# Optimization experiments

Hardware: AMD Instinct MI355X
Metric: run time of the kernel (lower is better)

Reference implementation:

```python
import jax, jax.numpy as jnp
import numpy as np

RETURN_SHAPE = (128, 128)


def dht2(x):
    # Discrete Hartley Transform over the spatial axes (2, 3):
    # H = Re(FFT) - Im(FFT). Unnormalized, matching scipy.fft default.
    f = jnp.fft.fftn(x, axes=(2, 3))
    return f.real - f.imag


def setup_inputs() -> dict:
    key = jax.random.key(0)
    x = jax.random.normal(key, (8, 64, 256, 256), dtype=jnp.float32)
    return {"x": x}


def reference(x) -> jnp.ndarray:
    # Spectral pooling: DHT -> center crop in frequency domain -> DHT.
    h_out, w_out = RETURN_SHAPE
    H, W = x.shape[2], x.shape[3]
    d = dht2(x)
    sh = (H - h_out) // 2
    sw = (W - w_out) // 2
    cropped = d[:, :, sh:sh + h_out, sw:sw + w_out]
    return dht2(cropped).astype(jnp.float32)
```

## Files before the change

kernel.cpp:

```cpp
#include <hip/hip_runtime.h>
#include <math.h>


typedef __attribute__((ext_vector_type(8))) short bfrag;
typedef __attribute__((ext_vector_type(4))) float ffrag;

#define PI2_256 0.0245436926061702597f
#define PI2_128 0.0490873852123405194f

__device__ __forceinline__ unsigned short f2bf(float f) {
    union { float f; unsigned int u; } v; v.f = f;
    unsigned int r = v.u + 0x7fffu + ((v.u >> 16) & 1u);
    return (unsigned short)(r >> 16);
}

__device__ __forceinline__ bfrag pack8(float4 a, float4 b) {
    bfrag r;
    r[0] = (short)f2bf(a.x); r[1] = (short)f2bf(a.y);
    r[2] = (short)f2bf(a.z); r[3] = (short)f2bf(a.w);
    r[4] = (short)f2bf(b.x); r[5] = (short)f2bf(b.y);
    r[6] = (short)f2bf(b.z); r[7] = (short)f2bf(b.w);
    return r;
}

__global__ __launch_bounds__(256) void gen_tables(unsigned short* __restrict__ ws)
{
    const int id = blockIdx.x * 256 + threadIdx.x;
    {
        const int j = id >> 8, m = id & 255;
        const int mult = (j < 128) ? (64 + j) : (320 - j);
        const int idx = (mult * m) & 255;
        float s, c; sincosf((float)idx * PI2_256, &s, &c);
        ws[id] = f2bf(c + s);
    }
    {
        const int u = id >> 9, k = id & 511;
        const int up = 64 + u;
        float s, c, val;
        if (k < 256) { sincosf((float)((up * k) & 255) * PI2_256, &s, &c); val = c; }
        else         { sincosf((float)((up * (k - 256)) & 255) * PI2_256, &s, &c); val = s; }
        ws[65536 + id] = f2bf(val);
    }
    if (id < 32768) {
        {
            const int j = id >> 7, m = id & 127;
            const int mult = (j < 128) ? j : (256 - j);
            const int idx = (mult * m) & 127;
            float s, c; sincosf((float)idx * PI2_128, &s, &c);
            ws[131072 + id] = f2bf(c + s);
        }
        {
            const int u = id >> 8, k = id & 255;
            float s, c, val;
            if (k < 128) { sincosf((float)((u * k) & 127) * PI2_128, &s, &c); val = c; }
            else         { sincosf((float)((u * (k - 128)) & 127) * PI2_128, &s, &c); val = s; }
            ws[163840 + id] = f2bf(val);
        }
    }
}

__global__ __launch_bounds__(512, 2) void stage1(const float* __restrict__ X,
                                                 const unsigned short* __restrict__ ws,
                                                 float* __restrict__ dc)
{
    __shared__ unsigned short PQt[128 * 512];

    const int t  = threadIdx.x;
    const int w  = t >> 6;
    const int ln = t & 15;
    const int q  = (t & 63) >> 4;
    const int img = blockIdx.x;

    const float* __restrict__ Xi = X + (size_t)img * 65536;
    const unsigned short* __restrict__ W1 = ws;
    const unsigned short* __restrict__ W2 = ws + 65536;

    {
        ffrag acc[2][16];
#pragma unroll
        for (int mt = 0; mt < 2; ++mt)
#pragma unroll
            for (int nt = 0; nt < 16; ++nt)
                acc[mt][nt] = (ffrag){0.f, 0.f, 0.f, 0.f};

        const int rowA0 = 32 * w;
        for (int kk = 0; kk < 8; ++kk) {
            const int k = kk * 32 + q * 8;
            bfrag A[2];
#pragma unroll
            for (int mt = 0; mt < 2; ++mt) {
                const float* xp = Xi + (size_t)(rowA0 + 16 * mt + ln) * 256 + k;
                const float4 x0 = *(const float4*)xp;
                const float4 x1 = *(const float4*)(xp + 4);
                A[mt] = pack8(x0, x1);
            }
#pragma unroll
            for (int nt = 0; nt < 16; ++nt) {
                const int j = nt * 16 + ln;
                const bfrag B = *(const bfrag*)(W1 + j * 256 + k);
#pragma unroll
                for (int mt = 0; mt < 2; ++mt)
                    acc[mt][nt] = __builtin_amdgcn_mfma_f32_16x16x32_bf16(A[mt], B, acc[mt][nt], 0, 0, 0);
            }
        }
#pragma unroll
        for (int mt = 0; mt < 2; ++mt) {
#pragma unroll
            for (int nt = 0; nt < 16; ++nt) {
                const int c  = nt * 16 + ln;
                const int v  = c & 127;
                const int kb = ((c < 128) ? 0 : 256) + rowA0 + 16 * mt + 4 * q;
                const unsigned int lo = (unsigned int)f2bf(acc[mt][nt][0]) |
                                        ((unsigned int)f2bf(acc[mt][nt][1]) << 16);
                const unsigned int hi = (unsigned int)f2bf(acc[mt][nt][2]) |
                                        ((unsigned int)f2bf(acc[mt][nt][3]) << 16);
                const int phys = v * 512 + ((((kb >> 3) ^ (v & 7)) << 3)) + (kb & 7);
                *(uint2*)&PQt[phys] = make_uint2(lo, hi);
            }
        }
    }
    __syncthreads();

    {
        ffrag acc[8];
#pragma unroll
        for (int nt = 0; nt < 8; ++nt) acc[nt] = (ffrag){0.f, 0.f, 0.f, 0.f};

        const int u0 = 16 * w;
        for (int kk = 0; kk < 16; ++kk) {
            const int k = kk * 32 + q * 8;
            const bfrag A = *(const bfrag*)(W2 + (size_t)(u0 + ln) * 512 + k);
#pragma unroll
            for (int nt = 0; nt < 8; ++nt) {
                const int v = nt * 16 + ln;
                const int g = (k >> 3) ^ (v & 7);
                const bfrag B = *(const bfrag*)&PQt[v * 512 + (g << 3)];
                acc[nt] = __builtin_amdgcn_mfma_f32_16x16x32_bf16(A, B, acc[nt], 0, 0, 0);
            }
        }
        float* __restrict__ D = dc + (size_t)img * 16384;
#pragma unroll
        for (int nt = 0; nt < 8; ++nt) {
#pragma unroll
            for (int r = 0; r < 4; ++r) {
                const int u = u0 + 4 * q + r;
                const int v = nt * 16 + ln;
                D[u * 128 + v] = acc[nt][r];
            }
        }
    }
}

__global__ __launch_bounds__(256, 2) void stage2(const unsigned short* __restrict__ ws,
                                                 float* __restrict__ io)
{
    __shared__ unsigned short Dcb[128 * 128];
    __shared__ unsigned short PQ2[64 * 256];

    const int t  = threadIdx.x;
    const int w  = t >> 6;
    const int ln = t & 15;
    const int q  = (t & 63) >> 4;
    const int img = blockIdx.x;

    float* __restrict__ G = io + (size_t)img * 16384;
    const unsigned short* __restrict__ W3 = ws + 131072;
    const unsigned short* __restrict__ W4 = ws + 163840;

    {
        const int p = t >> 1, half = t & 1;
        const float* src = G + p * 128 + half * 64;
#pragma unroll
        for (int g = 0; g < 8; ++g) {
            const float4 a = *(const float4*)(src + g * 8);
            const float4 b = *(const float4*)(src + g * 8 + 4);
            const int m0 = half * 64 + g * 8;
            const int gran = (m0 >> 3) ^ (p & 7);
            uint4 val;
            val.x = (unsigned int)f2bf(a.x) | ((unsigned int)f2bf(a.y) << 16);
            val.y = (unsigned int)f2bf(a.z) | ((unsigned int)f2bf(a.w) << 16);
            val.z = (unsigned int)f2bf(b.x) | ((unsigned int)f2bf(b.y) << 16);
            val.w = (unsigned int)f2bf(b.z) | ((unsigned int)f2bf(b.w) << 16);
            *(uint4*)&Dcb[p * 128 + gran * 8] = val;
        }
    }
    __syncthreads();

    for (int vh = 0; vh < 2; ++vh) {
        ffrag acc[2][8];
#pragma unroll
        for (int mt = 0; mt < 2; ++mt)
#pragma unroll
            for (int nt = 0; nt < 8; ++nt)
                acc[mt][nt] = (ffrag){0.f, 0.f, 0.f, 0.f};

        const int p0 = 32 * w;
        for (int kk = 0; kk < 4; ++kk) {
            const int k = kk * 32 + q * 8;
            bfrag A[2];
#pragma unroll
            for (int mt = 0; mt < 2; ++mt) {
                const int p = p0 + 16 * mt + ln;
                const int g = (k >> 3) ^ (p & 7);
                A[mt] = *(const bfrag*)&Dcb[p * 128 + g * 8];
            }
#pragma unroll
            for (int nt = 0; nt < 8; ++nt) {
                const int c = nt * 16 + ln;
                const int j = (c < 64) ? (64 * vh + c) : (128 + 64 * vh + (c - 64));
                const bfrag B = *(const bfrag*)(W3 + j * 128 + k);
#pragma unroll
                for (int mt = 0; mt < 2; ++mt)
                    acc[mt][nt] = __builtin_amdgcn_mfma_f32_16x16x32_bf16(A[mt], B, acc[mt][nt], 0, 0, 0);
            }
        }
        __syncthreads();
#pragma unroll
        for (int mt = 0; mt < 2; ++mt) {
#pragma unroll
            for (int nt = 0; nt < 8; ++nt) {
                const int c  = nt * 16 + ln;
                const int v  = c & 63;
                const int kb = ((c < 64) ? 0 : 128) + p0 + 16 * mt + 4 * q;
                const unsigned int lo = (unsigned int)f2bf(acc[mt][nt][0]) |
                                        ((unsigned int)f2bf(acc[mt][nt][1]) << 16);
                const unsigned int hi = (unsigned int)f2bf(acc[mt][nt][2]) |
                                        ((unsigned int)f2bf(acc[mt][nt][3]) << 16);
                const int phys = v * 256 + ((((kb >> 3) ^ (v & 7)) << 3)) + (kb & 7);
                *(uint2*)&PQ2[phys] = make_uint2(lo, hi);
            }
        }
        __syncthreads();

        ffrag o[2][4];
#pragma unroll
        for (int mt = 0; mt < 2; ++mt)
#pragma unroll
            for (int nt = 0; nt < 4; ++nt)
                o[mt][nt] = (ffrag){0.f, 0.f, 0.f, 0.f};

        const int u0 = 32 * w;
        for (int kk = 0; kk < 8; ++kk) {
            const int k = kk * 32 + q * 8;
            bfrag A[2];
#pragma unroll
            for (int mt = 0; mt < 2; ++mt)
                A[mt] = *(const bfrag*)(W4 + (size_t)(u0 + 16 * mt + ln) * 256 + k);
#pragma unroll
            for (int nt = 0; nt < 4; ++nt) {
                const int v = nt * 16 + ln;
                const int g = (k >> 3) ^ (v & 7);
                const bfrag B = *(const bfrag*)&PQ2[v * 256 + (g << 3)];
#pragma unroll
                for (int mt = 0; mt < 2; ++mt)
                    o[mt][nt] = __builtin_amdgcn_mfma_f32_16x16x32_bf16(A[mt], B, o[mt][nt], 0, 0, 0);
            }
        }
#pragma unroll
        for (int mt = 0; mt < 2; ++mt) {
#pragma unroll
            for (int nt = 0; nt < 4; ++nt) {
#pragma unroll
                for (int r = 0; r < 4; ++r) {
                    const int u = u0 + 16 * mt + 4 * q + r;
                    const int v = 64 * vh + nt * 16 + ln;
                    G[u * 128 + v] = o[mt][nt][r];
                }
            }
        }
    }
}

extern "C" void kernel_launch(void* const* d_in, const int* in_sizes, int n_in,
                              void* d_out, int out_size, void* d_ws, size_t ws_size,
                              hipStream_t stream)
{
    const float* x = (const float*)d_in[0];
    float* out = (float*)d_out;
    unsigned short* tw = (unsigned short*)d_ws;

    gen_tables<<<dim3(256), dim3(256), 0, stream>>>(tw);
    stage1<<<dim3(512), dim3(512), 0, stream>>>(x, tw, out);
    stage2<<<dim3(512), dim3(256), 0, stream>>>(tw, out);
}
```

Measured before the change: 276.8 us.

## Exploit Hartley symmetry to halve first-pass DHT GEMM width and shrink LDS

The first pass (width direction) now computes only the 129 unique cas-basis columns instead of 256 paired columns. The second pass recovers the mirrored columns by reading the row at 128-v from shared memory, which removes nearly half of the first-pass MFMA work and halves the LDS footprint. Stage2 gets the same mirrored-read treatment, reads its input straight from global memory instead of staging it through LDS, and moves to 512 threads with fewer syncs. Occupancy hints rise to 4 blocks per CU. The risks are the extra index arithmetic and the wasted 9th N-tile (only one useful column).

```diff
diff --git a/kernel.cpp b/kernel.cpp
--- a/kernel.cpp
+++ b/kernel.cpp
@@ -27,95 +27,80 @@
 {
     const int id = blockIdx.x * 256 + threadIdx.x;
     {
-        const int j = id >> 8, m = id & 255;
-        const int mult = (j < 128) ? (64 + j) : (320 - j);
-        const int idx = (mult * m) & 255;
-        float s, c; sincosf((float)idx * PI2_256, &s, &c);
-        ws[id] = f2bf(c + s);
-    }
-    {
         const int u = id >> 9, k = id & 511;
         const int up = 64 + u;
         float s, c, val;
         if (k < 256) { sincosf((float)((up * k) & 255) * PI2_256, &s, &c); val = c; }
         else         { sincosf((float)((up * (k - 256)) & 255) * PI2_256, &s, &c); val = s; }
-        ws[65536 + id] = f2bf(val);
+        ws[36864 + id] = f2bf(val);
+    }
+    if (id < 36864) {
+        const int c = id >> 8, m = id & 255;
+        const int idx = ((64 + c) * m) & 255;
+        float s, cc; sincosf((float)idx * PI2_256, &s, &cc);
+        ws[id] = f2bf(cc + s);
+    }
+    if (id < 16384) {
+        const int c = id >> 7, m = id & 127;
+        const int idx = (c * m) & 127;
+        float s, cc; sincosf((float)idx * PI2_128, &s, &cc);
+        ws[102400 + id] = f2bf(cc + s);
     }
     if (id < 32768) {
-        {
-            const int j = id >> 7, m = id & 127;
-            const int mult = (j < 128) ? j : (256 - j);
-            const int idx = (mult * m) & 127;
-            float s, c; sincosf((float)idx * PI2_128, &s, &c);
-            ws[131072 + id] = f2bf(c + s);
-        }
-        {
-            const int u = id >> 8, k = id & 255;
-            float s, c, val;
-            if (k < 128) { sincosf((float)((u * k) & 127) * PI2_128, &s, &c); val = c; }
-            else         { sincosf((float)((u * (k - 128)) & 127) * PI2_128, &s, &c); val = s; }
-            ws[163840 + id] = f2bf(val);
-        }
-    }
-}
-
-__global__ __launch_bounds__(512, 2) void stage1(const float* __restrict__ X,
+        const int u = id >> 8, k = id & 255;
+        float s, c, val;
+        if (k < 128) { sincosf((float)((u * k) & 127) * PI2_128, &s, &c); val = c; }
+        else         { sincosf((float)((u * (k - 128)) & 127) * PI2_128, &s, &c); val = s; }
+        ws[118784 + id] = f2bf(val);
+    }
+}
+
+__global__ __launch_bounds__(512, 4) void stage1(const float* __restrict__ X,
                                                  const unsigned short* __restrict__ ws,
                                                  float* __restrict__ dc)
 {
-    __shared__ unsigned short PQt[128 * 512];
+    __shared__ unsigned short Pt[129 * 256];
 
     const int t  = threadIdx.x;
     const int w  = t >> 6;
     const int ln = t & 15;
     const int q  = (t & 63) >> 4;
-    const int img = blockIdx.x;
-
-    const float* __restrict__ Xi = X + (size_t)img * 65536;
+
+    const float* __restrict__ Xi = X + (size_t)blockIdx.x * 65536;
     const unsigned short* __restrict__ W1 = ws;
-    const unsigned short* __restrict__ W2 = ws + 65536;
-
-    {
-        ffrag acc[2][16];
-#pragma unroll
-        for (int mt = 0; mt < 2; ++mt)
-#pragma unroll
-            for (int nt = 0; nt < 16; ++nt)
-                acc[mt][nt] = (ffrag){0.f, 0.f, 0.f, 0.f};
-
-        const int rowA0 = 32 * w;
+    const unsigned short* __restrict__ W2 = ws + 36864;
+
+#pragma unroll
+    for (int rp = 0; rp < 2; ++rp) {
+        const int base = rp * 128 + w * 16;
+        ffrag acc[9];
+#pragma unroll
+        for (int nt = 0; nt < 9; ++nt) acc[nt] = (ffrag){0.f, 0.f, 0.f, 0.f};
+
+        const float* __restrict__ xrow = Xi + (size_t)(base + ln) * 256;
+#pragma unroll
         for (int kk = 0; kk < 8; ++kk) {
             const int k = kk * 32 + q * 8;
-            bfrag A[2];
-#pragma unroll
-            for (int mt = 0; mt < 2; ++mt) {
-                const float* xp = Xi + (size_t)(rowA0 + 16 * mt + ln) * 256 + k;
-                const float4 x0 = *(const float4*)xp;
-                const float4 x1 = *(const float4*)(xp + 4);
-                A[mt] = pack8(x0, x1);
-            }
-#pragma unroll
-            for (int nt = 0; nt < 16; ++nt) {
-                const int j = nt * 16 + ln;
-                const bfrag B = *(const bfrag*)(W1 + j * 256 + k);
-#pragma unroll
-                for (int mt = 0; mt < 2; ++mt)
-                    acc[mt][nt] = __builtin_amdgcn_mfma_f32_16x16x32_bf16(A[mt], B, acc[mt][nt], 0, 0, 0);
-            }
-        }
-#pragma unroll
-        for (int mt = 0; mt < 2; ++mt) {
-#pragma unroll
-            for (int nt = 0; nt < 16; ++nt) {
-                const int c  = nt * 16 + ln;
-                const int v  = c & 127;
-                const int kb = ((c < 128) ? 0 : 256) + rowA0 + 16 * mt + 4 * q;
-                const unsigned int lo = (unsigned int)f2bf(acc[mt][nt][0]) |
-                                        ((unsigned int)f2bf(acc[mt][nt][1]) << 16);
-                const unsigned int hi = (unsigned int)f2bf(acc[mt][nt][2]) |
-                                        ((unsigned int)f2bf(acc[mt][nt][3]) << 16);
-                const int phys = v * 512 + ((((kb >> 3) ^ (v & 7)) << 3)) + (kb & 7);
-                *(uint2*)&PQt[phys] = make_uint2(lo, hi);
+            const float4 x0 = *(const float4*)(xrow + k);
+            const float4 x1 = *(const float4*)(xrow + k + 4);
+            const bfrag A = pack8(x0, x1);
+#pragma unroll
+            for (int nt = 0; nt < 9; ++nt) {
+                const bfrag B = *(const bfrag*)(W1 + (nt * 16 + ln) * 256 + k);
+                acc[nt] = __builtin_amdgcn_mfma_f32_16x16x32_bf16(A, B, acc[nt], 0, 0, 0);
+            }
+        }
+        const int n0 = base + 4 * q;
+#pragma unroll
+        for (int nt = 0; nt < 9; ++nt) {
+            const int c = nt * 16 + ln;
+            if (nt < 8 || ln == 0) {
+                const unsigned int lo = (unsigned int)f2bf(acc[nt][0]) |
+                                        ((unsigned int)f2bf(acc[nt][1]) << 16);
+                const unsigned int hi = (unsigned int)f2bf(acc[nt][2]) |
+                                        ((unsigned int)f2bf(acc[nt][3]) << 16);
+                const int phys = c * 256 + (((n0 >> 3) ^ (c & 7)) << 3) + (n0 & 7);
+                *(uint2*)&Pt[phys] = make_uint2(lo, hi);
             }
         }
     }
@@ -126,146 +111,106 @@
 #pragma unroll
         for (int nt = 0; nt < 8; ++nt) acc[nt] = (ffrag){0.f, 0.f, 0.f, 0.f};
 
-        const int u0 = 16 * w;
+        const int u0 = w * 16;
+#pragma unroll
         for (int kk = 0; kk < 16; ++kk) {
             const int k = kk * 32 + q * 8;
             const bfrag A = *(const bfrag*)(W2 + (size_t)(u0 + ln) * 512 + k);
+            const bool loK = (kk < 8);
 #pragma unroll
             for (int nt = 0; nt < 8; ++nt) {
-                const int v = nt * 16 + ln;
-                const int g = (k >> 3) ^ (v & 7);
-                const bfrag B = *(const bfrag*)&PQt[v * 512 + (g << 3)];
+                const int v   = nt * 16 + ln;
+                const int row = loK ? v : (128 - v);
+                const int col = loK ? k : (k - 256);
+                const int phys = row * 256 + (((col >> 3) ^ (row & 7)) << 3);
+                const bfrag B = *(const bfrag*)&Pt[phys];
                 acc[nt] = __builtin_amdgcn_mfma_f32_16x16x32_bf16(A, B, acc[nt], 0, 0, 0);
             }
         }
-        float* __restrict__ D = dc + (size_t)img * 16384;
+        float* __restrict__ D = dc + (size_t)blockIdx.x * 16384;
 #pragma unroll
         for (int nt = 0; nt < 8; ++nt) {
 #pragma unroll
             for (int r = 0; r < 4; ++r) {
-                const int u = u0 + 4 * q + r;
-                const int v = nt * 16 + ln;
-                D[u * 128 + v] = acc[nt][r];
-            }
-        }
-    }
-}
-
-__global__ __launch_bounds__(256, 2) void stage2(const unsigned short* __restrict__ ws,
+                D[(u0 + 4 * q + r) * 128 + nt * 16 + ln] = acc[nt][r];
+            }
+        }
+    }
+}
+
+__global__ __launch_bounds__(512, 4) void stage2(const unsigned short* __restrict__ ws,
                                                  float* __restrict__ io)
 {
-    __shared__ unsigned short Dcb[128 * 128];
-    __shared__ unsigned short PQ2[64 * 256];
+    __shared__ unsigned short P2t[128 * 128];
 
     const int t  = threadIdx.x;
     const int w  = t >> 6;
     const int ln = t & 15;
     const int q  = (t & 63) >> 4;
-    const int img = blockIdx.x;
-
-    float* __restrict__ G = io + (size_t)img * 16384;
-    const unsigned short* __restrict__ W3 = ws + 131072;
-    const unsigned short* __restrict__ W4 = ws + 163840;
-
-    {
-        const int p = t >> 1, half = t & 1;
-        const float* src = G + p * 128 + half * 64;
-#pragma unroll
-        for (int g = 0; g < 8; ++g) {
-            const float4 a = *(const float4*)(src + g * 8);
-            const float4 b = *(const float4*)(src + g * 8 + 4);
-            const int m0 = half * 64 + g * 8;
-            const int gran = (m0 >> 3) ^ (p & 7);
-            uint4 val;
-            val.x = (unsigned int)f2bf(a.x) | ((unsigned int)f2bf(a.y) << 16);
-            val.y = (unsigned int)f2bf(a.z) | ((unsigned int)f2bf(a.w) << 16);
-            val.z = (unsigned int)f2bf(b.x) | ((unsigned int)f2bf(b.y) << 16);
-            val.w = (unsigned int)f2bf(b.z) | ((unsigned int)f2bf(b.w) << 16);
-            *(uint4*)&Dcb[p * 128 + gran * 8] = val;
+
+    float* __restrict__ G = io + (size_t)blockIdx.x * 16384;
+    const unsigned short* __restrict__ W3 = ws + 102400;
+    const unsigned short* __restrict__ W4 = ws + 118784;
+
+    {
+        ffrag acc[8];
+#pragma unroll
+        for (int nt = 0; nt < 8; ++nt) acc[nt] = (ffrag){0.f, 0.f, 0.f, 0.f};
+
+        const int p0 = w * 16;
+        const float* __restrict__ drow = G + (size_t)(p0 + ln) * 128;
+#pragma unroll
+        for (int kk = 0; kk < 4; ++kk) {
+            const int k = kk * 32 + q * 8;
+            const float4 x0 = *(const float4*)(drow + k);
+            const float4 x1 = *(const float4*)(drow + k + 4);
+            const bfrag A = pack8(x0, x1);
+#pragma unroll
+            for (int nt = 0; nt < 8; ++nt) {
+                const bfrag B = *(const bfrag*)(W3 + (nt * 16 + ln) * 128 + k);
+                acc[nt] = __builtin_amdgcn_mfma_f32_16x16x32_bf16(A, B, acc[nt], 0, 0, 0);
+            }
+        }
+        const int n0 = p0 + 4 * q;
+#pragma unroll
+        for (int nt = 0; nt < 8; ++nt) {
+            const int c = nt * 16 + ln;
+            const unsigned int lo = (unsigned int)f2bf(acc[nt][0]) |
+                                    ((unsigned int)f2bf(acc[nt][1]) << 16);
+            const unsigned int hi = (unsigned int)f2bf(acc[nt][2]) |
+                                    ((unsigned int)f2bf(acc[nt][3]) << 16);
+            const int phys = c * 128 + (((n0 >> 3) ^ (c & 7)) << 3) + (n0 & 7);
+            *(uint2*)&P2t[phys] = make_uint2(lo, hi);
         }
     }
     __syncthreads();
 
-    for (int vh = 0; vh < 2; ++vh) {
-        ffrag acc[2][8];
-#pragma unroll
-        for (int mt = 0; mt < 2; ++mt)
-#pragma unroll
-            for (int nt = 0; nt < 8; ++nt)
-                acc[mt][nt] = (ffrag){0.f, 0.f, 0.f, 0.f};
-
-        const int p0 = 32 * w;
-        for (int kk = 0; kk < 4; ++kk) {
-            const int k = kk * 32 + q * 8;
-            bfrag A[2];
-#pragma unroll
-            for (int mt = 0; mt < 2; ++mt) {
-                const int p = p0 + 16 * mt + ln;
-                const int g = (k >> 3) ^ (p & 7);
-                A[mt] = *(const bfrag*)&Dcb[p * 128 + g * 8];
-            }
+    {
+        ffrag o[8];
+#pragma unroll
+        for (int nt = 0; nt < 8; ++nt) o[nt] = (ffrag){0.f, 0.f, 0.f, 0.f};
+
+        const int u0 = w * 16;
+#pragma unroll
+        for (int kk = 0; kk < 8; ++kk) {
+            const int k = kk * 32 + q * 8;
+            const bfrag A = *(const bfrag*)(W4 + (size_t)(u0 + ln) * 256 + k);
+            const bool loK = (kk < 4);
 #pragma unroll
             for (int nt = 0; nt < 8; ++nt) {
-                const int c = nt * 16 + ln;
-                const int j = (c < 64) ? (64 * vh + c) : (128 + 64 * vh + (c - 64));
-                const bfrag B = *(const bfrag*)(W3 + j * 128 + k);
-#pragma unroll
-                for (int mt = 0; mt < 2; ++mt)
-                    acc[mt][nt] = __builtin_amdgcn_mfma_f32_16x16x32_bf16(A[mt], B, acc[mt][nt], 0, 0, 0);
-            }
-        }
-        __syncthreads();
-#pragma unroll
-        for (int mt = 0; mt < 2; ++mt) {
-#pragma unroll
-            for (int nt = 0; nt < 8; ++nt) {
-                const int c  = nt * 16 + ln;
-                const int v  = c & 63;
-                const int kb = ((c < 64) ? 0 : 128) + p0 + 16 * mt + 4 * q;
-                const unsigned int lo = (unsigned int)f2bf(acc[mt][nt][0]) |
-                                        ((unsigned int)f2bf(acc[mt][nt][1]) << 16);
-                const unsigned int hi = (unsigned int)f2bf(acc[mt][nt][2]) |
-                                        ((unsigned int)f2bf(acc[mt][nt][3]) << 16);
-                const int phys = v * 256 + ((((kb >> 3) ^ (v & 7)) << 3)) + (kb & 7);
-                *(uint2*)&PQ2[phys] = make_uint2(lo, hi);
-            }
-        }
-        __syncthreads();
-
-        ffrag o[2][4];
-#pragma unroll
-        for (int mt = 0; mt < 2; ++mt)
-#pragma unroll
-            for (int nt = 0; nt < 4; ++nt)
-                o[mt][nt] = (ffrag){0.f, 0.f, 0.f, 0.f};
-
-        const int u0 = 32 * w;
-        for (int kk = 0; kk < 8; ++kk) {
-            const int k = kk * 32 + q * 8;
-            bfrag A[2];
-#pragma unroll
-            for (int mt = 0; mt < 2; ++mt)
-                A[mt] = *(const bfrag*)(W4 + (size_t)(u0 + 16 * mt + ln) * 256 + k);
-#pragma unroll
-            for (int nt = 0; nt < 4; ++nt) {
-                const int v = nt * 16 + ln;
-                const int g = (k >> 3) ^ (v & 7);
-                const bfrag B = *(const bfrag*)&PQ2[v * 256 + (g << 3)];
-#pragma unroll
-                for (int mt = 0; mt < 2; ++mt)
-                    o[mt][nt] = __builtin_amdgcn_mfma_f32_16x16x32_bf16(A[mt], B, o[mt][nt], 0, 0, 0);
-            }
-        }
-#pragma unroll
-        for (int mt = 0; mt < 2; ++mt) {
-#pragma unroll
-            for (int nt = 0; nt < 4; ++nt) {
-#pragma unroll
-                for (int r = 0; r < 4; ++r) {
-                    const int u = u0 + 16 * mt + 4 * q + r;
-                    const int v = 64 * vh + nt * 16 + ln;
-                    G[u * 128 + v] = o[mt][nt][r];
-                }
+                const int v   = nt * 16 + ln;
+                const int row = loK ? v : ((128 - v) & 127);
+                const int col = loK ? k : (k - 128);
+                const int phys = row * 128 + (((col >> 3) ^ (row & 7)) << 3);
+                const bfrag B = *(const bfrag*)&P2t[phys];
+                o[nt] = __builtin_amdgcn_mfma_f32_16x16x32_bf16(A, B, o[nt], 0, 0, 0);
+            }
+        }
+#pragma unroll
+        for (int nt = 0; nt < 8; ++nt) {
+#pragma unroll
+            for (int r = 0; r < 4; ++r) {
+                G[(u0 + 4 * q + r) * 128 + nt * 16 + ln] = o[nt][r];
             }
         }
     }
@@ -281,5 +226,5 @@
 
     gen_tables<<<dim3(256), dim3(256), 0, stream>>>(tw);
     stage1<<<dim3(512), dim3(512), 0, stream>>>(x, tw, out);
-    stage2<<<dim3(512), dim3(256), 0, stream>>>(tw, out);
-}
+    stage2<<<dim3(512), dim3(512), 0, stream>>>(tw, out);
+}
```

Measured after the change: 299.7 us. +8.3%, slower.
